# Optimization experiments

Hardware: AMD Instinct MI355X
Metric: run time of the kernel (lower is better)

## Reference

```python
import jax, jax.numpy as jnp
import numpy as np
from jax import lax

H = 1024   # h_size
S = 8192   # sequence length
T = 48     # n_tokens
START = 46
END = 47
NEG = -10000.0


def setup_inputs() -> dict:
    key = jax.random.key(0)
    ks = jax.random.split(key, 13)
    f32 = jnp.float32
    sc = 0.05
    sentence = jax.random.normal(ks[0], (S, 1, H), dtype=f32)
    W_ih_f = jax.random.normal(ks[1], (4 * H, H), dtype=f32) * sc
    W_hh_f = jax.random.normal(ks[2], (4 * H, H), dtype=f32) * sc
    b_ih_f = jax.random.normal(ks[3], (4 * H,), dtype=f32) * sc
    b_hh_f = jax.random.normal(ks[4], (4 * H,), dtype=f32) * sc
    W_ih_b = jax.random.normal(ks[5], (4 * H, H), dtype=f32) * sc
    W_hh_b = jax.random.normal(ks[6], (4 * H, H), dtype=f32) * sc
    b_ih_b = jax.random.normal(ks[7], (4 * H,), dtype=f32) * sc
    b_hh_b = jax.random.normal(ks[8], (4 * H,), dtype=f32) * sc
    W_dense = jax.random.normal(ks[9], (T, 2 * H), dtype=f32) * sc
    b_dense = jax.random.normal(ks[10], (T,), dtype=f32) * sc
    transitions = jax.random.normal(ks[11], (T, T), dtype=f32)
    transitions = transitions.at[START, :].set(NEG).at[:, END].set(NEG)
    return dict(sentence=sentence,
                W_ih_f=W_ih_f, W_hh_f=W_hh_f, b_ih_f=b_ih_f, b_hh_f=b_hh_f,
                W_ih_b=W_ih_b, W_hh_b=W_hh_b, b_ih_b=b_ih_b, b_hh_b=b_hh_b,
                W_dense=W_dense, b_dense=b_dense, transitions=transitions)


def _lstm_dir(x, W_ih, W_hh, b_ih, b_hh):
    # x: (S, H) -> hidden states (S, H). PyTorch gate order: i, f, g, o.
    xi = x @ W_ih.T + (b_ih + b_hh)  # precompute input projection: (S, 4H)
    Hd = W_hh.shape[1]

    def step(carry, xt):
        h, c = carry
        g = xt + h @ W_hh.T
        i, f, gg, o = jnp.split(g, 4, axis=-1)
        i = jax.nn.sigmoid(i)
        f = jax.nn.sigmoid(f)
        gg = jnp.tanh(gg)
        o = jax.nn.sigmoid(o)
        c = f * c + i * gg
        h = o * jnp.tanh(c)
        return (h, c), h

    h0 = jnp.zeros((Hd,), x.dtype)
    _, hs = lax.scan(step, (h0, h0), xi)
    return hs


def _viterbi(feats, transitions):
    # feats: (S, T). Vectorized max-plus recurrence over the tag dimension.
    def step(fv, feat):
        nv = fv[None, :] + transitions          # (T, T): row = next_tag, col = prev_tag
        bptr = jnp.argmax(nv, axis=1)           # (T,) best previous tag per next_tag
        fv_new = jnp.max(nv, axis=1) + feat     # (T,)
        return fv_new, bptr

    fv0 = jnp.full((T,), NEG, feats.dtype).at[START].set(0.0)
    fv, bptrs = lax.scan(step, fv0, feats)      # bptrs: (S, T) int32
    terminal = fv + transitions[END]
    best_last = jnp.argmax(terminal)
    path_score = terminal[best_last]

    # Backtrack: tag_{t-1} = bptrs[t][tag_t]; reverse scan emits tags 0..S-1.
    def back(tag, bp):
        return bp[tag], tag

    _, best_path = lax.scan(back, best_last, bptrs, reverse=True)
    return path_score, best_path


def reference(sentence, W_ih_f, W_hh_f, b_ih_f, b_hh_f,
              W_ih_b, W_hh_b, b_ih_b, b_hh_b,
              W_dense, b_dense, transitions):
    x = sentence[:, 0, :]                               # (S, H), batch=1 squeezed
    hf = _lstm_dir(x, W_ih_f, W_hh_f, b_ih_f, b_hh_f)   # forward direction
    hb = _lstm_dir(x[::-1], W_ih_b, W_hh_b, b_ih_b, b_hh_b)[::-1]  # backward
    out = jnp.concatenate([hf, hb], axis=-1)            # (S, 2H)
    feats = out @ W_dense.T + b_dense                   # (S, T)
    path_score, best_path = _viterbi(feats, transitions)
    return path_score, best_path
```

## Files before the change

kernel.cpp:

```cpp
#include <hip/hip_runtime.h>

#define S_LEN 8192
#define HDIM 1024
#define TTAG 48
#define START_TAG 46
#define END_TAG 47
#define CHUNK 1024
#define NCHUNK 8
#define NSLOT 16

typedef float f4 __attribute__((ext_vector_type(4)));

#define ASM_LD8(o0,o1,o2,o3,o4,o5,o6,o7,p)                                    \
  asm volatile("global_load_dwordx4 %0, %8, off\n\t"                          \
               "global_load_dwordx4 %1, %8, off offset:16\n\t"                \
               "global_load_dwordx4 %2, %8, off offset:32\n\t"                \
               "global_load_dwordx4 %3, %8, off offset:48\n\t"                \
               "global_load_dwordx4 %4, %8, off offset:64\n\t"                \
               "global_load_dwordx4 %5, %8, off offset:80\n\t"                \
               "global_load_dwordx4 %6, %8, off offset:96\n\t"                \
               "global_load_dwordx4 %7, %8, off offset:112\n\t"               \
               "s_waitcnt vmcnt(0)"                                           \
               : "=v"(o0),"=v"(o1),"=v"(o2),"=v"(o3),                         \
                 "=v"(o4),"=v"(o5),"=v"(o6),"=v"(o7)                          \
               : "v"(p) : "memory")

#define ASM_POLL3(a0,a1,a2,p)                                                 \
  asm volatile("global_load_dwordx4 %0, %3, off sc0 sc1\n\t"                  \
               "global_load_dwordx4 %1, %3, off offset:16 sc0 sc1\n\t"        \
               "global_load_dwordx4 %2, %3, off offset:32 sc0 sc1\n\t"        \
               "s_waitcnt vmcnt(0)"                                           \
               : "=v"(a0),"=v"(a1),"=v"(a2) : "v"(p) : "memory")

#define ASM_ST_SC(p,v4)                                                       \
  asm volatile("global_store_dwordx4 %0, %1, off sc0 sc1"                     \
               :: "v"(p), "v"(v4) : "memory")

__device__ __forceinline__ void fma4(const f4 wv, const f4 hv, float& acc) {
    acc = fmaf(wv.x, hv.x, acc);
    acc = fmaf(wv.y, hv.y, acc);
    acc = fmaf(wv.z, hv.z, acc);
    acc = fmaf(wv.w, hv.w, acc);
}

__global__ __launch_bounds__(256) void wdt_kernel(const float* __restrict__ Wd,
                                                  float* __restrict__ WdT) {
    int idx = blockIdx.x * 256 + threadIdx.x;
    if (idx < TTAG * 2048) {
        int tag = idx >> 11;
        int k = idx & 2047;
        WdT[(size_t)k * TTAG + tag] = Wd[idx];
    }
}

__global__ __launch_bounds__(256) void gemm_xi(
    const float* __restrict__ x,
    const float* __restrict__ Wf, const float* __restrict__ Wb,
    const float* __restrict__ bihf, const float* __restrict__ bhhf,
    const float* __restrict__ bihb, const float* __restrict__ bhhb,
    float* __restrict__ xi_ring, int chunk) {
    const int dir = blockIdx.z;
    const float* __restrict__ W = dir ? Wb : Wf;
    const float* __restrict__ bih = dir ? bihb : bihf;
    const float* __restrict__ bhh = dir ? bhhb : bhhf;

    const int mloc0 = blockIdx.y * 64;
    const int m0 = (dir == 0 ? chunk * CHUNK : S_LEN - (chunk + 1) * CHUNK) + mloc0;
    const int n0 = blockIdx.x * 64;

    __shared__ float As[16][68];
    __shared__ float Bs[16][68];

    const int tid = threadIdx.x;
    const int tx = tid & 15, ty = tid >> 4;
    const int lrow = tid >> 2, lk = (tid & 3) * 4;

    float acc[4][4];
#pragma unroll
    for (int a = 0; a < 4; a++)
#pragma unroll
        for (int b = 0; b < 4; b++) acc[a][b] = 0.f;

    const float* aptr = x + (size_t)(m0 + lrow) * HDIM + lk;
    const float* bptr = W + (size_t)(n0 + lrow) * HDIM + lk;

    for (int k0 = 0; k0 < HDIM; k0 += 16) {
        float4 av = *(const float4*)(aptr + k0);
        float4 bv = *(const float4*)(bptr + k0);
        __syncthreads();
        As[lk + 0][lrow] = av.x; As[lk + 1][lrow] = av.y;
        As[lk + 2][lrow] = av.z; As[lk + 3][lrow] = av.w;
        Bs[lk + 0][lrow] = bv.x; Bs[lk + 1][lrow] = bv.y;
        Bs[lk + 2][lrow] = bv.z; Bs[lk + 3][lrow] = bv.w;
        __syncthreads();
#pragma unroll
        for (int kk = 0; kk < 16; kk++) {
            float4 a4 = *(const float4*)&As[kk][ty * 4];
            float4 b4 = *(const float4*)&Bs[kk][tx * 4];
            float a[4] = {a4.x, a4.y, a4.z, a4.w};
            float b[4] = {b4.x, b4.y, b4.z, b4.w};
#pragma unroll
            for (int ii = 0; ii < 4; ii++)
#pragma unroll
                for (int jj = 0; jj < 4; jj++)
                    acc[ii][jj] = fmaf(a[ii], b[jj], acc[ii][jj]);
        }
    }

    const int n = n0 + tx * 4;
    const int gate = n >> 10;
    const int sl = (n & 1023) >> 3;
    const int e0 = n & 7;
    float4 bias;
    bias.x = bih[n + 0] + bhh[n + 0];
    bias.y = bih[n + 1] + bhh[n + 1];
    bias.z = bih[n + 2] + bhh[n + 2];
    bias.w = bih[n + 3] + bhh[n + 3];

#pragma unroll
    for (int ii = 0; ii < 4; ii++) {
        int mloc = mloc0 + ty * 4 + ii;
        int iloc = dir ? (CHUNK - 1 - mloc) : mloc;
        float4 v;
        v.x = acc[ii][0] + bias.x;
        v.y = acc[ii][1] + bias.y;
        v.z = acc[ii][2] + bias.z;
        v.w = acc[ii][3] + bias.w;
        *(float4*)(xi_ring + ((size_t)(dir * 128 + sl) * CHUNK + iloc) * 32 + gate * 8 + e0) = v;
    }
}

__global__ __launch_bounds__(256, 1) void lstm_chunk(
    const float* __restrict__ xi_ring, float* __restrict__ hall,
    float* __restrict__ hrec, float* __restrict__ cstate,
    const float* __restrict__ Whhf, const float* __restrict__ Whhb, int chunk) {
    __shared__ float hsh[HDIM];
    __shared__ float psum[256];

    const int tid = threadIdx.x;
    const int bx = blockIdx.x;
    const int dir = bx >> 7;
    const int slice = bx & 127;
    const int row32 = tid & 31;
    const int kc = tid >> 5;
    const int gate = row32 >> 3;
    const int eloc = row32 & 7;

    const float* __restrict__ Whh = dir ? Whhb : Whhf;
    const int R = gate * HDIM + slice * 8 + eloc;
    const float* wsrc = Whh + (size_t)R * HDIM + kc * 128;

    f4 w00,w01,w02,w03,w04,w05,w06,w07,w08,w09,w10,w11,w12,w13,w14,w15;
    f4 w16,w17,w18,w19,w20,w21,w22,w23,w24,w25,w26,w27,w28,w29,w30,w31;
    ASM_LD8(w00,w01,w02,w03,w04,w05,w06,w07, wsrc);
    ASM_LD8(w08,w09,w10,w11,w12,w13,w14,w15, wsrc + 32);
    ASM_LD8(w16,w17,w18,w19,w20,w21,w22,w23, wsrc + 64);
    ASM_LD8(w24,w25,w26,w27,w28,w29,w30,w31, wsrc + 96);

    float creg = 0.f;
    if (chunk > 0 && tid < 8) creg = cstate[dir * HDIM + slice * 8 + tid];

    const size_t hbase = (size_t)dir * ((size_t)S_LEN * HDIM);
    f4* hsh4 = (f4*)hsh;

    for (int i = 0; i < CHUNK; i++) {
        const int t = chunk * CHUNK + i;

        float xi_v = 0.f;
        if (tid < 32) xi_v = xi_ring[((size_t)bx * CHUNK + (size_t)i) * 32 + tid];

        if (t == 0) {
            f4 z; z.x = 0.f; z.y = 0.f; z.z = 0.f; z.w = 0.f;
            hsh4[tid] = z;
        } else if (tid < 128) {
            const int j = (t - 1) & (NSLOT - 1);
            const float* rp = hrec + ((size_t)(dir * NSLOT + j) * 128 + tid) * 12;
            f4 a0, a1, a2;
            do {
                ASM_POLL3(a0, a1, a2, rp);
            } while (__float_as_int(a0.w) != t || __float_as_int(a1.w) != t ||
                     __float_as_int(a2.w) != t);
            f4 u, v;
            u.x = a0.x; u.y = a0.y; u.z = a0.z; u.w = a1.x;
            v.x = a1.y; v.y = a1.z; v.z = a2.x; v.w = a2.y;
            hsh4[2 * tid] = u;
            hsh4[2 * tid + 1] = v;
        }
        __syncthreads();

        float acc0 = 0.f, acc1 = 0.f, acc2 = 0.f, acc3 = 0.f;
        const f4* h4p = (const f4*)hsh + kc * 32;
        fma4(w00, h4p[0],  acc0); fma4(w01, h4p[1],  acc1);
        fma4(w02, h4p[2],  acc2); fma4(w03, h4p[3],  acc3);
        fma4(w04, h4p[4],  acc0); fma4(w05, h4p[5],  acc1);
        fma4(w06, h4p[6],  acc2); fma4(w07, h4p[7],  acc3);
        fma4(w08, h4p[8],  acc0); fma4(w09, h4p[9],  acc1);
        fma4(w10, h4p[10], acc2); fma4(w11, h4p[11], acc3);
        fma4(w12, h4p[12], acc0); fma4(w13, h4p[13], acc1);
        fma4(w14, h4p[14], acc2); fma4(w15, h4p[15], acc3);
        fma4(w16, h4p[16], acc0); fma4(w17, h4p[17], acc1);
        fma4(w18, h4p[18], acc2); fma4(w19, h4p[19], acc3);
        fma4(w20, h4p[20], acc0); fma4(w21, h4p[21], acc1);
        fma4(w22, h4p[22], acc2); fma4(w23, h4p[23], acc3);
        fma4(w24, h4p[24], acc0); fma4(w25, h4p[25], acc1);
        fma4(w26, h4p[26], acc2); fma4(w27, h4p[27], acc3);
        fma4(w28, h4p[28], acc0); fma4(w29, h4p[29], acc1);
        fma4(w30, h4p[30], acc2); fma4(w31, h4p[31], acc3);
        psum[kc * 32 + row32] = (acc0 + acc1) + (acc2 + acc3);
        __syncthreads();

        if (tid < 64) {
            const int l5 = tid & 31;
            float g = xi_v;
#pragma unroll
            for (int q = 0; q < 8; q++) g += psum[q * 32 + l5];
            const int e = tid & 7;
            float gI = __shfl(g, e);
            float gF = __shfl(g, 8 + e);
            float gG = __shfl(g, 16 + e);
            float gO = __shfl(g, 24 + e);
            float iv = 1.f / (1.f + expf(-gI));
            float fv = 1.f / (1.f + expf(-gF));
            float gv = tanhf(gG);
            float ov = 1.f / (1.f + expf(-gO));
            float cn = fv * creg + iv * gv;
            creg = cn;
            float hv = ov * tanhf(cn);

            float h0 = __shfl(hv, 0), h1 = __shfl(hv, 1), h2 = __shfl(hv, 2);
            float h3 = __shfl(hv, 3), h4 = __shfl(hv, 4), h5 = __shfl(hv, 5);
            float h6 = __shfl(hv, 6), h7 = __shfl(hv, 7);

            if (tid < 8)
                hall[hbase + (size_t)t * HDIM + slice * 8 + tid] = hv;
            if (tid < 3) {
                f4 av;
                av.x = (tid == 0) ? h0 : (tid == 1) ? h3 : h6;
                av.y = (tid == 0) ? h1 : (tid == 1) ? h4 : h7;
                av.z = (tid == 0) ? h2 : (tid == 1) ? h5 : h7;
                av.w = __int_as_float(t + 1);
                float* sp = hrec +
                    ((size_t)(dir * NSLOT + (t & (NSLOT - 1))) * 128 + slice) * 12 +
                    tid * 4;
                ASM_ST_SC(sp, av);
            }
        }
    }

    if (tid < 8) cstate[dir * HDIM + slice * 8 + tid] = creg;
}

__global__ __launch_bounds__(256) void feats_kernel(
    const float* __restrict__ hall, const float* __restrict__ WdT,
    const float* __restrict__ bd, float* __restrict__ feats) {
    __shared__ float hsh[2048];
    __shared__ float red[TTAG * 256];
    __shared__ float red2[192];

    const int t = blockIdx.x;
    const int tid = threadIdx.x;

    ((float4*)hsh)[tid] = ((const float4*)(hall + (size_t)t * HDIM))[tid];
    ((float4*)hsh)[256 + tid] =
        ((const float4*)(hall + (size_t)S_LEN * HDIM + (size_t)(S_LEN - 1 - t) * HDIM))[tid];
    __syncthreads();

    float acc[TTAG];
#pragma unroll
    for (int j = 0; j < TTAG; j++) acc[j] = 0.f;

    const int kbase = tid * 8;
#pragma unroll
    for (int q = 0; q < 8; q++) {
        float hv = hsh[kbase + q];
        const float4* wr = (const float4*)(WdT + (size_t)(kbase + q) * TTAG);
#pragma unroll
        for (int p = 0; p < 12; p++) {
            float4 w = wr[p];
            acc[p * 4 + 0] = fmaf(hv, w.x, acc[p * 4 + 0]);
            acc[p * 4 + 1] = fmaf(hv, w.y, acc[p * 4 + 1]);
            acc[p * 4 + 2] = fmaf(hv, w.z, acc[p * 4 + 2]);
            acc[p * 4 + 3] = fmaf(hv, w.w, acc[p * 4 + 3]);
        }
    }
#pragma unroll
    for (int j = 0; j < TTAG; j++) red[j * 256 + tid] = acc[j];
    __syncthreads();

    if (tid < 192) {
        int tag = tid >> 2, p = tid & 3;
        float s = 0.f;
#pragma unroll
        for (int q = 0; q < 64; q++) s += red[tag * 256 + p * 64 + q];
        red2[tag * 4 + p] = s;
    }
    __syncthreads();

    if (tid < TTAG) {
        feats[(size_t)t * TTAG + tid] =
            red2[tid * 4] + red2[tid * 4 + 1] + red2[tid * 4 + 2] + red2[tid * 4 + 3] + bd[tid];
    }
}

__global__ __launch_bounds__(64, 1) void viterbi_kernel(
    const float* __restrict__ feats, const float* __restrict__ trans,
    unsigned char* __restrict__ bp, float* __restrict__ out) {
    __shared__ float fbuf[2][64 * TTAG];
    __shared__ float fvsh[64];
    const int lane = threadIdx.x;

    float tr[TTAG];
#pragma unroll
    for (int j = 0; j < TTAG; j++)
        tr[j] = (lane < TTAG) ? trans[lane * TTAG + j] : -3.0e38f;

    fvsh[lane] = (lane == START_TAG) ? 0.0f
               : (lane < TTAG) ? -10000.0f : -3.0e38f;

    const f4* f4src = (const f4*)feats;
    f4 nx[12];
#pragma unroll
    for (int q = 0; q < 12; q++) nx[q] = f4src[q * 64 + lane];
    {
        f4* nb = (f4*)fbuf[0];
#pragma unroll
        for (int q = 0; q < 12; q++) nb[q * 64 + lane] = nx[q];
    }
    __syncthreads();

    for (int blk = 0; blk < 128; blk++) {
        const float* fb = fbuf[blk & 1];
        if (blk < 127) {
#pragma unroll
            for (int q = 0; q < 12; q++)
                nx[q] = f4src[(size_t)(blk + 1) * 768 + q * 64 + lane];
        }

        for (int step = 0; step < 64; step++) {
            const int t = blk * 64 + step;
            float feat = (lane < TTAG) ? fb[step * TTAG + lane] : 0.f;

            float fvv[TTAG];
#pragma unroll
            for (int jj = 0; jj < 12; jj++) {
                f4 v4 = *(const f4*)&fvsh[jj * 4];
                fvv[jj * 4 + 0] = v4.x; fvv[jj * 4 + 1] = v4.y;
                fvv[jj * 4 + 2] = v4.z; fvv[jj * 4 + 3] = v4.w;
            }

            float v[64];
            int ix[64];
#pragma unroll
            for (int j = 0; j < TTAG; j++) { v[j] = fvv[j] + tr[j]; ix[j] = j; }
#pragma unroll
            for (int j = TTAG; j < 64; j++) { v[j] = -3.0e38f; ix[j] = j; }

#pragma unroll
            for (int len = 64; len > 1; len >>= 1) {
#pragma unroll
                for (int q = 0; q < (len >> 1); q++) {
                    bool tb = v[2 * q + 1] > v[2 * q];
                    v[q] = tb ? v[2 * q + 1] : v[2 * q];
                    ix[q] = tb ? ix[2 * q + 1] : ix[2 * q];
                }
            }

            if (lane < TTAG) bp[(size_t)t * TTAG + lane] = (unsigned char)ix[0];
            float nfv = (lane < TTAG) ? (v[0] + feat) : -3.0e38f;
            fvsh[lane] = nfv;
        }

        if (blk < 127) {
            f4* nb = (f4*)fbuf[(blk + 1) & 1];
#pragma unroll
            for (int q = 0; q < 12; q++) nb[q * 64 + lane] = nx[q];
        }
        __syncthreads();
    }

    float term = (lane < TTAG) ? fvsh[lane] + trans[END_TAG * TTAG + lane]
                               : -3.0e38f;
    __syncthreads();
    fvsh[lane] = term;
    __syncthreads();
    int bl = 0;
    if (lane == 0) {
        float best = -3.4e38f;
        for (int i = 0; i < TTAG; i++) {
            if (fvsh[i] > best) { best = fvsh[i]; bl = i; }
        }
        out[0] = best;
    }
    int tag = __shfl(bl, 0);
    if (lane == 0) out[1 + S_LEN - 1] = (float)tag;

    for (int rb = S_LEN - 1; rb >= 1; rb -= 48) {
        const int jmax = (rb < 48) ? rb : 48;
        int bval[48];
#pragma unroll
        for (int j = 0; j < 48; j++)
            bval[j] = (j < jmax) ? (int)bp[(size_t)(rb - j) * TTAG + lane] : 0;
#pragma unroll
        for (int j = 0; j < 48; j++) {
            if (j < jmax) {
                tag = __shfl(bval[j], tag);
                if (lane == 0) out[rb - j] = (float)tag;
            }
        }
    }
}

extern "C" void kernel_launch(void* const* d_in, const int* in_sizes, int n_in,
                              void* d_out, int out_size, void* d_ws, size_t ws_size,
                              hipStream_t stream) {
    const float* sent = (const float*)d_in[0];
    const float* Wihf = (const float*)d_in[1];
    const float* Whhf = (const float*)d_in[2];
    const float* bihf = (const float*)d_in[3];
    const float* bhhf = (const float*)d_in[4];
    const float* Wihb = (const float*)d_in[5];
    const float* Whhb = (const float*)d_in[6];
    const float* bihb = (const float*)d_in[7];
    const float* bhhb = (const float*)d_in[8];
    const float* Wd = (const float*)d_in[9];
    const float* bd = (const float*)d_in[10];
    const float* trans = (const float*)d_in[11];
    float* out = (float*)d_out;

    float* ws = (float*)d_ws;
    float* xi_ring = ws;
    float* hall = ws + 8388608;
    float* hrec = hall + 16777216;
    float* cstate = hrec + 49152;
    float* featsb = cstate + 2048;
    float* wdT = featsb + 393216;
    unsigned char* bp = (unsigned char*)(wdT + 98304);

    wdt_kernel<<<dim3(384), dim3(256), 0, stream>>>(Wd, wdT);

    for (int c = 0; c < NCHUNK; c++) {
        gemm_xi<<<dim3(64, 16, 2), dim3(256), 0, stream>>>(
            sent, Wihf, Wihb, bihf, bhhf, bihb, bhhb, xi_ring, c);
        lstm_chunk<<<dim3(256), dim3(256), 0, stream>>>(
            xi_ring, hall, hrec, cstate, Whhf, Whhb, c);
    }

    feats_kernel<<<dim3(8192), dim3(256), 0, stream>>>(hall, wdT, bd, featsb);
    viterbi_kernel<<<dim3(1), dim3(64), 0, stream>>>(featsb, trans, bp, out);
}
```

Baseline: 30.19 ms.

## Parallelize Viterbi forward pass via segmented max-plus matrix products

Replaces the single-wave sequential Viterbi forward recurrence over 8192 steps with a three-phase parallel scheme. First, 256 blocks each build the 48x48 max-plus transfer matrix for a 32-step segment. Next, one wave scans the 256 segment matrices to get the score vector at each segment boundary. Finally, 256 blocks replay their segments in parallel from those seeds to write backpointers. This removes the long serial critical path, at the cost of extra max-plus matrix work, workspace traffic, and possible float-reassociation differences in ties or argmax.

```diff
diff --git a/kernel.cpp b/kernel.cpp
--- a/kernel.cpp
+++ b/kernel.cpp
@@ -8,6 +8,8 @@
 #define CHUNK 1024
 #define NCHUNK 8
 #define NSLOT 16
+#define VSEG 256
+#define VLEN 32
 
 typedef float f4 __attribute__((ext_vector_type(4)));
 
@@ -302,87 +304,190 @@
     }
 }
 
-__global__ __launch_bounds__(64, 1) void viterbi_kernel(
+__global__ __launch_bounds__(256) void vit_products(
     const float* __restrict__ feats, const float* __restrict__ trans,
-    unsigned char* __restrict__ bp, float* __restrict__ out) {
-    __shared__ float fbuf[2][64 * TTAG];
+    float* __restrict__ Pseg) {
+    __shared__ float PL[2][TTAG * TTAG];
+    __shared__ float fsh[VLEN * TTAG];
+
+    const int tid = threadIdx.x;
+    const int seg = blockIdx.x;
+    const int lane = tid & 63;
+    const int wave = tid >> 6;
+    const int i = lane;
+    const int ir = (i < TTAG) ? i : (TTAG - 1);
+
+    const f4* ft = (const f4*)(feats + (size_t)seg * VLEN * TTAG);
+    for (int q = tid; q < VLEN * TTAG / 4; q += 256)
+        ((f4*)fsh)[q] = ft[q];
+
+    float tr[TTAG];
+#pragma unroll
+    for (int k4 = 0; k4 < 12; k4++) {
+        f4 v = ((const f4*)(trans + ir * TTAG))[k4];
+        tr[k4 * 4 + 0] = v.x; tr[k4 * 4 + 1] = v.y;
+        tr[k4 * 4 + 2] = v.z; tr[k4 * 4 + 3] = v.w;
+    }
+    __syncthreads();
+
+    if (i < TTAG) {
+        float f0 = fsh[i];
+#pragma unroll
+        for (int j12 = 0; j12 < 12; j12++) {
+            int j = wave * 12 + j12;
+            PL[0][j * TTAG + i] = trans[ir * TTAG + j] + f0;
+        }
+    }
+    __syncthreads();
+
+    int cur = 0;
+    for (int step = 1; step < VLEN; step++) {
+        const float* PLc = PL[cur];
+        float* PLn = PL[cur ^ 1];
+        float fstep = fsh[step * TTAG + ir];
+#pragma unroll
+        for (int j12 = 0; j12 < 12; j12++) {
+            int j = wave * 12 + j12;
+            const f4* pc = (const f4*)(PLc + j * TTAG);
+            float m = -3.0e38f;
+#pragma unroll
+            for (int k4 = 0; k4 < 12; k4++) {
+                f4 p = pc[k4];
+                m = fmaxf(m, fmaxf(fmaxf(tr[k4 * 4 + 0] + p.x, tr[k4 * 4 + 1] + p.y),
+                                   fmaxf(tr[k4 * 4 + 2] + p.z, tr[k4 * 4 + 3] + p.w)));
+            }
+            if (i < TTAG) PLn[j * TTAG + i] = fstep + m;
+        }
+        cur ^= 1;
+        __syncthreads();
+    }
+
+    if (i < TTAG) {
+        float* outp = Pseg + (size_t)seg * (TTAG * TTAG) + i * TTAG;
+#pragma unroll
+        for (int k4 = 0; k4 < 3; k4++) {
+            int k = wave * 12 + k4 * 4;
+            f4 v;
+            v.x = PL[cur][(k + 0) * TTAG + i];
+            v.y = PL[cur][(k + 1) * TTAG + i];
+            v.z = PL[cur][(k + 2) * TTAG + i];
+            v.w = PL[cur][(k + 3) * TTAG + i];
+            *(f4*)(outp + k) = v;
+        }
+    }
+}
+
+__global__ __launch_bounds__(64) void vit_scan(
+    const float* __restrict__ Pseg, float* __restrict__ seeds) {
     __shared__ float fvsh[64];
     const int lane = threadIdx.x;
+    const int lr = (lane < TTAG) ? lane : (TTAG - 1);
+
+    float fv = (lane == START_TAG) ? 0.f
+             : (lane < TTAG) ? -10000.f : -3.0e38f;
+    fvsh[lane] = fv;
+
+    f4 pr[12], nx[12];
+    const f4* rp0 = (const f4*)(Pseg + (size_t)lr * TTAG);
+#pragma unroll
+    for (int q = 0; q < 12; q++) pr[q] = rp0[q];
+
+    for (int s = 0; s < VSEG; s++) {
+        if (lane < TTAG) seeds[s * TTAG + lane] = fv;
+        if (s < VSEG - 1) {
+            const f4* np = (const f4*)(Pseg + (size_t)(s + 1) * (TTAG * TTAG) + lr * TTAG);
+#pragma unroll
+            for (int q = 0; q < 12; q++) nx[q] = np[q];
+        }
+        float fvv[TTAG];
+#pragma unroll
+        for (int jj = 0; jj < 12; jj++) {
+            f4 v4 = *(const f4*)&fvsh[jj * 4];
+            fvv[jj * 4 + 0] = v4.x; fvv[jj * 4 + 1] = v4.y;
+            fvv[jj * 4 + 2] = v4.z; fvv[jj * 4 + 3] = v4.w;
+        }
+        float m = -3.0e38f;
+#pragma unroll
+        for (int q = 0; q < 12; q++) {
+            f4 p = pr[q];
+            m = fmaxf(m, fmaxf(fmaxf(p.x + fvv[q * 4 + 0], p.y + fvv[q * 4 + 1]),
+                               fmaxf(p.z + fvv[q * 4 + 2], p.w + fvv[q * 4 + 3])));
+        }
+        fv = (lane < TTAG) ? m : -3.0e38f;
+        fvsh[lane] = fv;
+#pragma unroll
+        for (int q = 0; q < 12; q++) pr[q] = nx[q];
+    }
+    if (lane < TTAG) seeds[VSEG * TTAG + lane] = fv;
+}
+
+__global__ __launch_bounds__(64) void vit_replay(
+    const float* __restrict__ feats, const float* __restrict__ trans,
+    const float* __restrict__ seeds, unsigned char* __restrict__ bp) {
+    __shared__ float fsh[VLEN * TTAG];
+    __shared__ float fvsh[64];
+    const int lane = threadIdx.x;
+    const int seg = blockIdx.x;
 
     float tr[TTAG];
 #pragma unroll
     for (int j = 0; j < TTAG; j++)
         tr[j] = (lane < TTAG) ? trans[lane * TTAG + j] : -3.0e38f;
 
-    fvsh[lane] = (lane == START_TAG) ? 0.0f
-               : (lane < TTAG) ? -10000.0f : -3.0e38f;
-
-    const f4* f4src = (const f4*)feats;
-    f4 nx[12];
-#pragma unroll
-    for (int q = 0; q < 12; q++) nx[q] = f4src[q * 64 + lane];
-    {
-        f4* nb = (f4*)fbuf[0];
-#pragma unroll
-        for (int q = 0; q < 12; q++) nb[q * 64 + lane] = nx[q];
-    }
-    __syncthreads();
-
-    for (int blk = 0; blk < 128; blk++) {
-        const float* fb = fbuf[blk & 1];
-        if (blk < 127) {
-#pragma unroll
-            for (int q = 0; q < 12; q++)
-                nx[q] = f4src[(size_t)(blk + 1) * 768 + q * 64 + lane];
-        }
-
-        for (int step = 0; step < 64; step++) {
-            const int t = blk * 64 + step;
-            float feat = (lane < TTAG) ? fb[step * TTAG + lane] : 0.f;
-
-            float fvv[TTAG];
-#pragma unroll
-            for (int jj = 0; jj < 12; jj++) {
-                f4 v4 = *(const f4*)&fvsh[jj * 4];
-                fvv[jj * 4 + 0] = v4.x; fvv[jj * 4 + 1] = v4.y;
-                fvv[jj * 4 + 2] = v4.z; fvv[jj * 4 + 3] = v4.w;
+    const f4* ft = (const f4*)(feats + (size_t)seg * VLEN * TTAG);
+#pragma unroll
+    for (int q = 0; q < 6; q++) ((f4*)fsh)[q * 64 + lane] = ft[q * 64 + lane];
+
+    fvsh[lane] = (lane < TTAG) ? seeds[seg * TTAG + lane] : -3.0e38f;
+    __syncthreads();
+
+    for (int step = 0; step < VLEN; step++) {
+        const int t = seg * VLEN + step;
+        float feat = (lane < TTAG) ? fsh[step * TTAG + lane] : 0.f;
+
+        float fvv[TTAG];
+#pragma unroll
+        for (int jj = 0; jj < 12; jj++) {
+            f4 v4 = *(const f4*)&fvsh[jj * 4];
+            fvv[jj * 4 + 0] = v4.x; fvv[jj * 4 + 1] = v4.y;
+            fvv[jj * 4 + 2] = v4.z; fvv[jj * 4 + 3] = v4.w;
+        }
+
+        float v[64];
+        int ix[64];
+#pragma unroll
+        for (int j = 0; j < TTAG; j++) { v[j] = fvv[j] + tr[j]; ix[j] = j; }
+#pragma unroll
+        for (int j = TTAG; j < 64; j++) { v[j] = -3.0e38f; ix[j] = j; }
+
+#pragma unroll
+        for (int len = 64; len > 1; len >>= 1) {
+#pragma unroll
+            for (int q = 0; q < (len >> 1); q++) {
+                bool tb = v[2 * q + 1] > v[2 * q];
+                v[q] = tb ? v[2 * q + 1] : v[2 * q];
+                ix[q] = tb ? ix[2 * q + 1] : ix[2 * q];
             }
-
-            float v[64];
-            int ix[64];
-#pragma unroll
-            for (int j = 0; j < TTAG; j++) { v[j] = fvv[j] + tr[j]; ix[j] = j; }
-#pragma unroll
-            for (int j = TTAG; j < 64; j++) { v[j] = -3.0e38f; ix[j] = j; }
-
-#pragma unroll
-            for (int len = 64; len > 1; len >>= 1) {
-#pragma unroll
-                for (int q = 0; q < (len >> 1); q++) {
-                    bool tb = v[2 * q + 1] > v[2 * q];
-                    v[q] = tb ? v[2 * q + 1] : v[2 * q];
-                    ix[q] = tb ? ix[2 * q + 1] : ix[2 * q];
-                }
-            }
-
-            if (lane < TTAG) bp[(size_t)t * TTAG + lane] = (unsigned char)ix[0];
-            float nfv = (lane < TTAG) ? (v[0] + feat) : -3.0e38f;
-            fvsh[lane] = nfv;
-        }
-
-        if (blk < 127) {
-            f4* nb = (f4*)fbuf[(blk + 1) & 1];
-#pragma unroll
-            for (int q = 0; q < 12; q++) nb[q * 64 + lane] = nx[q];
-        }
-        __syncthreads();
-    }
-
-    float term = (lane < TTAG) ? fvsh[lane] + trans[END_TAG * TTAG + lane]
-                               : -3.0e38f;
-    __syncthreads();
+        }
+
+        if (lane < TTAG) bp[(size_t)t * TTAG + lane] = (unsigned char)ix[0];
+        float nfv = (lane < TTAG) ? (v[0] + feat) : -3.0e38f;
+        fvsh[lane] = nfv;
+    }
+}
+
+__global__ __launch_bounds__(64) void vit_backtrace(
+    const float* __restrict__ seeds, const float* __restrict__ trans,
+    const unsigned char* __restrict__ bp, float* __restrict__ out) {
+    __shared__ float fvsh[64];
+    const int lane = threadIdx.x;
+
+    float term = (lane < TTAG)
+        ? seeds[VSEG * TTAG + lane] + trans[END_TAG * TTAG + lane]
+        : -3.0e38f;
     fvsh[lane] = term;
     __syncthreads();
+
     int bl = 0;
     if (lane == 0) {
         float best = -3.4e38f;
@@ -435,6 +540,8 @@
     float* featsb = cstate + 2048;
     float* wdT = featsb + 393216;
     unsigned char* bp = (unsigned char*)(wdT + 98304);
+    float* Pseg = wdT + 98304 + 98304;
+    float* seeds = Pseg + 589824;
 
     wdt_kernel<<<dim3(384), dim3(256), 0, stream>>>(Wd, wdT);
 
@@ -446,5 +553,9 @@
     }
 
     feats_kernel<<<dim3(8192), dim3(256), 0, stream>>>(hall, wdT, bd, featsb);
-    viterbi_kernel<<<dim3(1), dim3(64), 0, stream>>>(featsb, trans, bp, out);
-}
+
+    vit_products<<<dim3(VSEG), dim3(256), 0, stream>>>(featsb, trans, Pseg);
+    vit_scan<<<dim3(1), dim3(64), 0, stream>>>(Pseg, seeds);
+    vit_replay<<<dim3(VSEG), dim3(64), 0, stream>>>(featsb, trans, seeds, bp);
+    vit_backtrace<<<dim3(1), dim3(64), 0, stream>>>(seeds, trans, bp, out);
+}
```

After: 26.13 ms. 13.5% less time.
